# Performance work log

Measured on AMD Instinct MI355X. Metric: run time of the kernel, lower is better.

Reference implementation:

```python
import jax, jax.numpy as jnp
import numpy as np


def setup_inputs() -> dict:
    key = jax.random.key(0)
    ks = jax.random.split(key, 5)
    B, C, H, W = 32, 2048, 14, 14
    K = 113  # num_concepts + 1
    NUM_CLASSES = 200
    x = jax.random.normal(ks[0], (B, C, H, W), dtype=jnp.float32)
    concepts = jax.random.normal(ks[1], (K, C), dtype=jnp.float32)
    # small init scale for linear heads (keeps sigmoid/logits in a sane range)
    concept_fc_w = jax.random.normal(ks[2], (1, C), dtype=jnp.float32) * 0.02
    concept_fc_b = jnp.zeros((1,), dtype=jnp.float32)
    label_fc_w = jax.random.normal(ks[3], (NUM_CLASSES, C), dtype=jnp.float32) * 0.02
    label_fc_b = jnp.zeros((NUM_CLASSES,), dtype=jnp.float32)
    return {
        "x": x,
        "concepts": concepts,
        "concept_fc_w": concept_fc_w,
        "concept_fc_b": concept_fc_b,
        "label_fc_w": label_fc_w,
        "label_fc_b": label_fc_b,
    }


def reference(x, concepts, concept_fc_w, concept_fc_b, label_fc_w, label_fc_b):
    b, c, h, w = x.shape
    h2, w2 = h * 2, w * 2
    # F.interpolate(mode='bilinear', align_corners=False) == jax.image.resize bilinear
    x = jax.image.resize(x, (b, c, h2, w2), method="bilinear")
    xe = x.reshape(b, c, h2 * w2).transpose(0, 2, 1)  # [b, n, c]
    # cdist(concepts, xe, p=2) via matmul expansion (matches torch's mm-based cdist)
    x_sq = jnp.sum(xe * xe, axis=-1)                    # [b, n]
    c_sq = jnp.sum(concepts * concepts, axis=-1)        # [k]
    dots = jnp.einsum("kc,bnc->bkn", concepts, xe)      # [b, k, n]
    d2 = c_sq[None, :, None] + x_sq[:, None, :] - 2.0 * dots
    dists = jnp.sqrt(jnp.maximum(d2, 0.0))              # [b, k, n]
    attn = jax.nn.softmax(-dists, axis=1)               # softmax over concepts
    score_maps = attn.reshape(b, -1, h2, w2)            # [b, k, h2, w2]
    concept_vecs = jnp.einsum("bkn,bnc->bkc", attn[:, :-1, :], xe)  # [b, k-1, c]
    logits = jnp.einsum("bkc,c->bk", concept_vecs, concept_fc_w[0]) + concept_fc_b[0]
    concept_scores = jax.nn.sigmoid(logits)             # [b, k-1]
    preds = (concept_scores @ concepts[:-1, :]) @ label_fc_w.T + label_fc_b  # [b, 200]
    return score_maps, concept_scores, preds
```

## Files before the change

kernel.cpp:

```cpp
#include <hip/hip_runtime.h>
#include <hip/hip_bf16.h>
#include <cstdint>

typedef __attribute__((ext_vector_type(8))) short short8;
typedef __attribute__((ext_vector_type(4))) float f32x4;
typedef __attribute__((ext_vector_type(16))) float f32x16;

#define BDIM 32
#define CDIM 2048
#define NPIX 196
#define HIN 14
#define N2 784
#define W2 28
#define KDIM 113
#define KC 112
#define NCLS 200
#define NBX 14
#define BNC 56
#define NSTEP 64
#define PST 224
#define GST 200
#define RDST 68
#define SSTB 60

__global__ __launch_bounds__(256) void k_prep(const float* __restrict__ concepts,
                                              const float* __restrict__ cfcw,
                                              ushort* __restrict__ cbf,
                                              float* __restrict__ csq) {
  int k = blockIdx.x, t = threadIdx.x;
  const int kt = k >> 5, row = k & 31;
  float s = 0.f;
  for (int c = t; c < CDIM; c += 256) {
    float v = (k < KDIM) ? concepts[(size_t)k * CDIM + c] : (k == KDIM ? cfcw[c] : 0.f);
    __hip_bfloat16 h = __float2bfloat16(v);
    int st = c >> 5, it = (c >> 4) & 1, g2 = (c >> 3) & 1, j = c & 7;
    cbf[(((size_t)st * 4 + kt) * 2 + it) * 512 + (g2 * 32 + row) * 8 + j] = __bfloat16_as_ushort(h);
    float vb = __bfloat162float(h);
    s = fmaf(vb, vb, s);
  }
  __shared__ float r[4];
#pragma unroll
  for (int off = 32; off > 0; off >>= 1) s += __shfl_down(s, off, 64);
  if ((t & 63) == 0) r[t >> 6] = s;
  __syncthreads();
  if (t == 0) csq[k] = r[0] + r[1] + r[2] + r[3];
}

__global__ __launch_bounds__(512, 4) void k_xt(const float* __restrict__ x,
                                               ushort* __restrict__ xt,
                                               float* __restrict__ Gpart) {
  __shared__ float P[2][32 * PST];
  const int sg = blockIdx.x, b = blockIdx.y;
  const int tid = threadIdx.x;
  const int lane = tid & 63, wv = tid >> 6;
  const int chg = tid >> 4, seg = tid & 15;
  const int p0 = seg * 13;

  const int c0a = tid / 49,           pq0 = tid - c0a * 49;
  const int c1a = (tid + 512) / 49,   pq1 = (tid + 512) - c1a * 49;
  const int c2a = (tid + 1024) / 49,  pq2 = (tid + 1024) - c2a * 49;
  const int c3a = (tid + 1536) / 49,  pq3 = (tid + 1536) - c3a * 49;

  for (int z = tid; z < 2 * 32 * 28; z += 512) {
    int buf = z / 896, r = z - buf * 896;
    int c = r / 28, j = r - c * 28;
    P[buf][c * PST + 196 + j] = 0.f;
  }

  float g[13][5];
#pragma unroll
  for (int p = 0; p < 13; ++p)
#pragma unroll
    for (int t = 0; t < 5; ++t) g[p][t] = 0.f;

  float4 q0, q1, q2, q3 = {0.f, 0.f, 0.f, 0.f};
  auto LOADQ = [&](int s) {
    const float4* src = (const float4*)(x + ((size_t)b * CDIM + s * 32) * NPIX);
    q0 = src[tid]; q1 = src[tid + 512]; q2 = src[tid + 1024];
    if (tid < 32) q3 = src[tid + 1536];
  };
  auto WRITEQ = [&](int buf) {
    float* Pb = P[buf];
    *(float4*)&Pb[c0a * PST + 4 * pq0] = q0;
    *(float4*)&Pb[c1a * PST + 4 * pq1] = q1;
    *(float4*)&Pb[c2a * PST + 4 * pq2] = q2;
    if (tid < 32) *(float4*)&Pb[c3a * PST + 4 * pq3] = q3;
  };

  LOADQ(sg * 4);
  WRITEQ(0);
  __syncthreads();

  for (int si = 0; si < 4; ++si) {
    const int s = sg * 4 + si;
    const int cur = si & 1;
    if (si < 3) LOADQ(s + 1);
#pragma unroll
    for (int pass = 0; pass < 2; ++pass) {
      int slot = tid + pass * 512;
      if (slot < 896) {
        int t = slot >> 7, r = slot & 127;
        int it = r >> 6, l = r & 63;
        int pxp = t * 32 + (l & 31);
        int row = pxp >> 4, col = pxp & 15;
        int c0 = it * 16 + (l >> 5) * 8;
        uint uu[4];
        if (col < 14) {
          int px = row * HIN + col;
#pragma unroll
          for (int p = 0; p < 4; ++p) {
            float v0 = P[cur][(c0 + 2 * p) * PST + px];
            float v1 = P[cur][(c0 + 2 * p + 1) * PST + px];
            uu[p] = (uint)__bfloat16_as_ushort(__float2bfloat16(v0)) |
                    ((uint)__bfloat16_as_ushort(__float2bfloat16(v1)) << 16);
          }
        } else {
          uu[0] = uu[1] = uu[2] = uu[3] = 0u;
        }
        uint4 pk; pk.x = uu[0]; pk.y = uu[1]; pk.z = uu[2]; pk.w = uu[3];
        *(uint4*)&xt[((((size_t)b * 7 + t) * 64 + s) * 1024) + it * 512 + (size_t)l * 8] = pk;
      }
    }
    {
      float xv[28];
      const float* Pr = &P[cur][chg * PST];
#pragma unroll
      for (int i = 0; i < 7; ++i) *(float4*)&xv[4 * i] = *(const float4*)&Pr[p0 + 4 * i];
#pragma unroll
      for (int p = 0; p < 13; ++p) {
        float a = xv[p];
        g[p][0] = fmaf(a, a, g[p][0]);
        g[p][1] = fmaf(a, xv[p + 1], g[p][1]);
        g[p][2] = fmaf(a, xv[p + 13], g[p][2]);
        g[p][3] = fmaf(a, xv[p + 14], g[p][3]);
        g[p][4] = fmaf(a, xv[p + 15], g[p][4]);
      }
    }
    if (si < 3) WRITEQ((si + 1) & 1);
    __syncthreads();
  }

  float* Gw = &P[0][0];
#pragma unroll
  for (int p = 0; p < 13; ++p)
#pragma unroll
    for (int t = 0; t < 5; ++t) {
      float v = g[p][t];
      v += __shfl_xor(v, 16, 64);
      v += __shfl_xor(v, 32, 64);
      g[p][t] = v;
    }
  if (lane < 16) {
#pragma unroll
    for (int p = 0; p < 13; ++p)
#pragma unroll
      for (int t = 0; t < 5; ++t) Gw[((size_t)wv * 16 + lane) * 65 + p * 5 + t] = g[p][t];
  }
  __syncthreads();
#pragma unroll
  for (int it = 0; it < 2; ++it) {
    int slot = tid + it * 512;
    if (slot < 16 * 65) {
      int sseg = slot / 65, i = slot - sseg * 65;
      float v = 0.f;
#pragma unroll
      for (int ww = 0; ww < 8; ++ww) v += Gw[((size_t)ww * 16 + sseg) * 65 + i];
      int pl = i / 5, ty = i - pl * 5;
      int px = sseg * 13 + pl;
      if (px < NPIX)
        Gpart[((size_t)b * 16 + sg) * (5 * GST) + ty * GST + px] = v;
    }
  }
}

__global__ __launch_bounds__(256) void k_gred(const float* __restrict__ Gpart,
                                              float* __restrict__ Gs) {
  const int b = blockIdx.x, tid = threadIdx.x;
  for (int i = tid; i < 5 * GST; i += 256) {
    float v = 0.f;
#pragma unroll
    for (int sg = 0; sg < 16; ++sg) v += Gpart[((size_t)b * 16 + sg) * (5 * GST) + i];
    Gs[(size_t)b * (5 * GST) + i] = v;
  }
}

__global__ __launch_bounds__(256, 3) void k_gemm3(
    const ushort* __restrict__ xt,
    const ushort* __restrict__ cbf,
    const float* __restrict__ Gs,
    const float* __restrict__ csq,
    float* __restrict__ attn_out,
    float* __restrict__ part)
{
  __shared__ float RDs[128 * RDST];
  __shared__ ushort Ssb[KDIM * SSTB];
  __shared__ float csq_s[KDIM];
  __shared__ float xsqs[BNC], projs2[BNC];

  const int tid = threadIdx.x;
  const int wgid = blockIdx.x;
  const int xcd = wgid & 7, slot = wgid >> 3;
  const int bq = slot / NBX, bx = slot - bq * NBX;
  const int b = xcd + 8 * bq;
  const int n0 = bx * BNC;
  const int lane = tid & 63, w = tid >> 6;

  int r0 = bx - 1; if (r0 < 0) r0 = 0; if (r0 > 11) r0 = 11;
  const int T0 = r0 >> 1;

  if (tid < KDIM) csq_s[tid] = csq[tid];

  const ushort* abp = cbf + w * 1024 + lane * 8;
  const ushort* xtb = xt + (((size_t)b * 7 + T0) << 16) + lane * 8;

  f32x16 acc[2];
#pragma unroll
  for (int tt = 0; tt < 2; ++tt)
#pragma unroll
    for (int r = 0; r < 16; ++r) acc[tt][r] = 0.f;

#define LOADSET(A_, B_, S_)                                              \
  do {                                                                   \
    const size_t so_ = (size_t)(S_) * 4096;                              \
    const size_t xo_ = (size_t)(S_) * 1024;                              \
    A_[0] = *(const uint4*)(abp + so_);                                  \
    A_[1] = *(const uint4*)(abp + so_ + 512);                            \
    B_[0][0] = *(const uint4*)(xtb + xo_);                               \
    B_[0][1] = *(const uint4*)(xtb + xo_ + 512);                         \
    B_[1][0] = *(const uint4*)(xtb + 65536 + xo_);                       \
    B_[1][1] = *(const uint4*)(xtb + 65536 + xo_ + 512);                 \
  } while (0)

#define COMPUTE(A_, B_)                                                  \
  do {                                                                   \
    _Pragma("unroll")                                                    \
    for (int it_ = 0; it_ < 2; ++it_) {                                  \
      short8 af_ = *(const short8*)&A_[it_];                             \
      acc[0] = __builtin_amdgcn_mfma_f32_32x32x16_bf16(                  \
          af_, *(const short8*)&B_[0][it_], acc[0], 0, 0, 0);            \
      acc[1] = __builtin_amdgcn_mfma_f32_32x32x16_bf16(                  \
          af_, *(const short8*)&B_[1][it_], acc[1], 0, 0, 0);            \
    }                                                                    \
  } while (0)

  uint4 a0[2], a1[2], b0[2][2], b1[2][2];
  LOADSET(a0, b0, 0);
  for (int s = 0; s < NSTEP; s += 2) {
    if (s + 1 < NSTEP) LOADSET(a1, b1, s + 1);
    COMPUTE(a0, b0);
    if (s + 2 < NSTEP) LOADSET(a0, b0, s + 2);
    COMPUTE(a1, b1);
  }
#undef LOADSET
#undef COMPUTE

#pragma unroll
  for (int tt = 0; tt < 2; ++tt)
#pragma unroll
    for (int r = 0; r < 16; ++r) {
      int row = w * 32 + (r & 3) + 8 * (r >> 2) + 4 * (lane >> 5);
      RDs[row * RDST + tt * 32 + (lane & 31)] = acc[tt][r];
    }
  __syncthreads();

  auto COLW = [&](int col, int& p1, int& p3, int& p1g, int& p3g,
                  float& w00, float& w01, float& w10, float& w11) {
    const int i2 = 2 * bx + (col >= 28 ? 1 : 0);
    const int j2 = col - (col >= 28 ? 28 : 0);
    float si = 0.5f * i2 - 0.25f, sj = 0.5f * j2 - 0.25f;
    float fif = floorf(si), fjf = floorf(sj);
    int ii = (int)fif, jj = (int)fjf;
    float fi = si - fif, fj = sj - fjf;
    int ia = ii < 0 ? 0 : ii; int ib = (ii + 1 > 13) ? 13 : ii + 1;
    int ja = jj < 0 ? 0 : jj; int jb = (jj + 1 > 13) ? 13 : jj + 1;
    w00 = (1.f - fi) * (1.f - fj); w01 = (1.f - fi) * fj;
    w10 = fi * (1.f - fj);         w11 = fi * fj;
    if (ib == ia) { w00 += w10; w01 += w11; w10 = 0.f; w11 = 0.f; }
    if (jb == ja) { w00 += w01; w10 += w11; w01 = 0.f; w11 = 0.f; }
    p1g = ia * HIN + ja; p3g = ib * HIN + ja;
    p1 = ia * 16 + ja - T0 * 32; p3 = ib * 16 + ja - T0 * 32;
  };

  if (tid < BNC) {
    int p1, p3, p1g, p3g; float w00, w01, w10, w11;
    COLW(tid, p1, p3, p1g, p3g, w00, w01, w10, w11);
    const float* Gb = Gs + (size_t)b * (5 * GST);
    const float* Gd = Gb, *Gr = Gb + GST, *Gy = Gb + 2 * GST, *Gv = Gb + 3 * GST, *Gx = Gb + 4 * GST;
    float xsq = w00 * w00 * Gd[p1g] + w01 * w01 * Gd[p1g + 1]
              + w10 * w10 * Gd[p3g] + w11 * w11 * Gd[p3g + 1]
              + 2.f * (w00 * w01 * Gr[p1g] + w10 * w11 * Gr[p3g]
                     + w00 * w10 * Gv[p1g] + w01 * w11 * Gv[p1g + 1]
                     + w00 * w11 * Gx[p1g] + w01 * w10 * Gy[p1g + 1]);
    const float* rp = &RDs[113 * RDST];
    float pj = w00 * rp[p1] + w01 * rp[p1 + 1] + w10 * rp[p3] + w11 * rp[p3 + 1];
    xsqs[tid] = xsq; projs2[tid] = pj;
  }
  __syncthreads();

  if (tid < BNC * 4) {
    const int col = tid >> 2, sub = tid & 3;
    int p1, p3, p1g, p3g; float w00, w01, w10, w11;
    COLW(col, p1, p3, p1g, p3g, w00, w01, w10, w11);
    const float xq = xsqs[col];
    float ev[29];
    float mx = -1e30f;
#pragma unroll
    for (int i = 0; i < 29; ++i) {
      int k = sub + 4 * i;
      if (k < KDIM) {
        const float* rk = &RDs[k * RDST];
        float dot = w00 * rk[p1] + w01 * rk[p1 + 1] + w10 * rk[p3] + w11 * rk[p3 + 1];
        float d2 = csq_s[k] + xq - 2.f * dot;
        float sv = -sqrtf(fmaxf(d2, 0.f));
        ev[i] = sv;
        mx = fmaxf(mx, sv);
      }
    }
    mx = fmaxf(mx, __shfl_xor(mx, 1, 64));
    mx = fmaxf(mx, __shfl_xor(mx, 2, 64));
    float ssum = 0.f;
#pragma unroll
    for (int i = 0; i < 29; ++i) {
      int k = sub + 4 * i;
      if (k < KDIM) {
        float e = __expf(ev[i] - mx);
        ev[i] = e;
        Ssb[k * SSTB + col] = __bfloat16_as_ushort(__float2bfloat16(e));
        ssum += e;
      }
    }
    ssum += __shfl_xor(ssum, 1, 64);
    ssum += __shfl_xor(ssum, 2, 64);
    const float rinv = 1.f / ssum;
    float* op = attn_out + (size_t)b * KDIM * N2 + n0 + col;
#pragma unroll
    for (int i = 0; i < 29; ++i) {
      int k = sub + 4 * i;
      if (k < KDIM) op[(size_t)k * N2] = ev[i] * rinv;
    }
    if (sub == 0) projs2[col] *= rinv;
  }
  __syncthreads();

  if (tid < KC * 2) {
    const int k = tid >> 1, s2 = tid & 1;
    float lg = 0.f;
    for (int c2 = s2; c2 < BNC; c2 += 2)
      lg = fmaf(__uint_as_float((uint)Ssb[k * SSTB + c2] << 16), projs2[c2], lg);
    lg += __shfl_xor(lg, 1, 64);
    if (s2 == 0) part[((size_t)b * NBX + bx) * KC + k] = lg;
  }
}

__global__ __launch_bounds__(256) void k_tmp(
    const float* __restrict__ concepts, const float* __restrict__ part,
    const float* __restrict__ cfcb, float* __restrict__ cs_out,
    float* __restrict__ tmp) {
  __shared__ float cs_s[KC];
  const int b = blockIdx.y, cx = blockIdx.x;
  const int t = threadIdx.x;
  if (t < KC) {
    float l = cfcb[0];
#pragma unroll
    for (int q = 0; q < NBX; ++q) l += part[((size_t)b * NBX + q) * KC + t];
    float csv = 1.f / (1.f + __expf(-l));
    cs_s[t] = csv;
    if (cx == 0) cs_out[b * KC + t] = csv;
  }
  __syncthreads();
  const int c = cx * 256 + t;
  float a = 0.f;
#pragma unroll 8
  for (int k = 0; k < KC; ++k) a = fmaf(cs_s[k], concepts[(size_t)k * CDIM + c], a);
  tmp[(size_t)b * CDIM + c] = a;
}

__global__ __launch_bounds__(256) void k_pred2(
    const float* __restrict__ labw, const float* __restrict__ labb,
    const float* __restrict__ tmp, float* __restrict__ preds) {
  const int w = blockIdx.x * 4 + (threadIdx.x >> 6);
  const int lane = threadIdx.x & 63;
  const int b = w / NCLS, cls = w % NCLS;
  if (b >= BDIM) return;
  const float* tr = tmp + (size_t)b * CDIM;
  const float* wr = labw + (size_t)cls * CDIM;
  float a = 0.f;
#pragma unroll
  for (int c0 = 0; c0 < CDIM; c0 += 256) {
    float4 t = *(const float4*)&tr[c0 + lane * 4];
    float4 v = *(const float4*)&wr[c0 + lane * 4];
    a += t.x * v.x + t.y * v.y + t.z * v.z + t.w * v.w;
  }
#pragma unroll
  for (int off = 32; off > 0; off >>= 1) a += __shfl_down(a, off, 64);
  if (lane == 0) preds[b * NCLS + cls] = a + labb[cls];
}

extern "C" void kernel_launch(void* const* d_in, const int* in_sizes, int n_in,
                              void* d_out, int out_size, void* d_ws, size_t ws_size,
                              hipStream_t stream) {
  const float* x        = (const float*)d_in[0];
  const float* concepts = (const float*)d_in[1];
  const float* cfcw     = (const float*)d_in[2];
  const float* cfcb     = (const float*)d_in[3];
  const float* labw     = (const float*)d_in[4];
  const float* labb     = (const float*)d_in[5];

  float* out    = (float*)d_out;
  float* sm_out = out;
  float* cs_out = out + (size_t)BDIM * KDIM * N2;
  float* pr_out = cs_out + (size_t)BDIM * KC;

  char* ws = (char*)d_ws;
  float*  csq   = (float*)(ws + 0);
  float*  part  = (float*)(ws + 512);
  ushort* cbf   = (ushort*)(ws + 201216);
  float*  tmp   = (float*)(ws + 725504);
  float*  Gpart = (float*)(ws + 987648);
  float*  Gs    = (float*)(ws + 3035648);
  ushort* xt    = (ushort*)(ws + 3163648);

  k_prep <<<dim3(128), dim3(256), 0, stream>>>(concepts, cfcw, cbf, csq);
  k_xt   <<<dim3(16, BDIM), dim3(512), 0, stream>>>(x, xt, Gpart);
  k_gred <<<dim3(BDIM), dim3(256), 0, stream>>>(Gpart, Gs);
  k_gemm3<<<dim3(448), dim3(256), 0, stream>>>(xt, cbf, Gs, csq, sm_out, part);
  k_tmp  <<<dim3(CDIM / 256, BDIM), dim3(256), 0, stream>>>(concepts, part, cfcb, cs_out, tmp);
  k_pred2<<<dim3((BDIM * NCLS + 3) / 4), dim3(256), 0, stream>>>(labw, labb, tmp, pr_out);
}
```

Measured before the change: 84.64 us.

## Merge prep and transpose kernels, fold G reduction into GEMM, deepen load pipeline

Combines the concept-prep and x-transpose kernels into one launch by giving extra workgroups the prep work. It drops the separate G-reduction kernel, so the GEMM kernel sums the 16 partials itself when it computes xsq. The GEMM main loop now prefetches four stages of registers instead of two. These changes cut two kernel launches and their sync points, and hide more global-load latency. In exchange the GEMM does more scattered global reads in its epilogue, and the deeper prefetch raises register pressure, which could lower occupancy. The stage kernel's launch bounds also drop from 4 to 2 blocks per CU.

```diff
diff --git a/kernel.cpp b/kernel.cpp
--- a/kernel.cpp
+++ b/kernel.cpp
@@ -23,36 +23,46 @@
 #define RDST 68
 #define SSTB 60
 
-__global__ __launch_bounds__(256) void k_prep(const float* __restrict__ concepts,
-                                              const float* __restrict__ cfcw,
-                                              ushort* __restrict__ cbf,
-                                              float* __restrict__ csq) {
-  int k = blockIdx.x, t = threadIdx.x;
-  const int kt = k >> 5, row = k & 31;
-  float s = 0.f;
-  for (int c = t; c < CDIM; c += 256) {
-    float v = (k < KDIM) ? concepts[(size_t)k * CDIM + c] : (k == KDIM ? cfcw[c] : 0.f);
-    __hip_bfloat16 h = __float2bfloat16(v);
-    int st = c >> 5, it = (c >> 4) & 1, g2 = (c >> 3) & 1, j = c & 7;
-    cbf[(((size_t)st * 4 + kt) * 2 + it) * 512 + (g2 * 32 + row) * 8 + j] = __bfloat16_as_ushort(h);
-    float vb = __bfloat162float(h);
-    s = fmaf(vb, vb, s);
-  }
-  __shared__ float r[4];
-#pragma unroll
-  for (int off = 32; off > 0; off >>= 1) s += __shfl_down(s, off, 64);
-  if ((t & 63) == 0) r[t >> 6] = s;
-  __syncthreads();
-  if (t == 0) csq[k] = r[0] + r[1] + r[2] + r[3];
-}
-
-__global__ __launch_bounds__(512, 4) void k_xt(const float* __restrict__ x,
-                                               ushort* __restrict__ xt,
-                                               float* __restrict__ Gpart) {
+__global__ __launch_bounds__(512, 2) void k_stage(
+    const float* __restrict__ x,
+    const float* __restrict__ concepts,
+    const float* __restrict__ cfcw,
+    ushort* __restrict__ cbf,
+    float* __restrict__ csq,
+    ushort* __restrict__ xt,
+    float* __restrict__ Gpart) {
   __shared__ float P[2][32 * PST];
-  const int sg = blockIdx.x, b = blockIdx.y;
+  __shared__ float r8[8];
+  const int wgid = blockIdx.x;
   const int tid = threadIdx.x;
   const int lane = tid & 63, wv = tid >> 6;
+
+  if (wgid >= 512) {
+    const int k = wgid - 512;
+    const int kt = k >> 5, row = k & 31;
+    float s = 0.f;
+    for (int c = tid; c < CDIM; c += 512) {
+      float v = (k < KDIM) ? concepts[(size_t)k * CDIM + c] : (k == KDIM ? cfcw[c] : 0.f);
+      __hip_bfloat16 h = __float2bfloat16(v);
+      int st = c >> 5, it = (c >> 4) & 1, g2 = (c >> 3) & 1, j = c & 7;
+      cbf[(((size_t)st * 4 + kt) * 2 + it) * 512 + (g2 * 32 + row) * 8 + j] = __bfloat16_as_ushort(h);
+      float vb = __bfloat162float(h);
+      s = fmaf(vb, vb, s);
+    }
+#pragma unroll
+    for (int off = 32; off > 0; off >>= 1) s += __shfl_down(s, off, 64);
+    if (lane == 0) r8[wv] = s;
+    __syncthreads();
+    if (tid == 0) {
+      float tot = 0.f;
+#pragma unroll
+      for (int i = 0; i < 8; ++i) tot += r8[i];
+      csq[k] = tot;
+    }
+    return;
+  }
+
+  const int sg = wgid & 15, b = wgid >> 4;
   const int chg = tid >> 4, seg = tid & 15;
   const int p0 = seg * 13;
 
@@ -173,21 +183,10 @@
   }
 }
 
-__global__ __launch_bounds__(256) void k_gred(const float* __restrict__ Gpart,
-                                              float* __restrict__ Gs) {
-  const int b = blockIdx.x, tid = threadIdx.x;
-  for (int i = tid; i < 5 * GST; i += 256) {
-    float v = 0.f;
-#pragma unroll
-    for (int sg = 0; sg < 16; ++sg) v += Gpart[((size_t)b * 16 + sg) * (5 * GST) + i];
-    Gs[(size_t)b * (5 * GST) + i] = v;
-  }
-}
-
 __global__ __launch_bounds__(256, 3) void k_gemm3(
     const ushort* __restrict__ xt,
     const ushort* __restrict__ cbf,
-    const float* __restrict__ Gs,
+    const float* __restrict__ Gpart,
     const float* __restrict__ csq,
     float* __restrict__ attn_out,
     float* __restrict__ part)
@@ -243,13 +242,17 @@
     }                                                                    \
   } while (0)
 
-  uint4 a0[2], a1[2], b0[2][2], b1[2][2];
-  LOADSET(a0, b0, 0);
-  for (int s = 0; s < NSTEP; s += 2) {
-    if (s + 1 < NSTEP) LOADSET(a1, b1, s + 1);
-    COMPUTE(a0, b0);
-    if (s + 2 < NSTEP) LOADSET(a0, b0, s + 2);
-    COMPUTE(a1, b1);
+  uint4 aA[2], aB[2], aC[2], aD[2];
+  uint4 bA[2][2], bB[2][2], bC[2][2], bD[2][2];
+  LOADSET(aA, bA, 0);
+  LOADSET(aB, bB, 1);
+  LOADSET(aC, bC, 2);
+  LOADSET(aD, bD, 3);
+  for (int s = 0; s < NSTEP; s += 4) {
+    COMPUTE(aA, bA); if (s + 4 < NSTEP) LOADSET(aA, bA, s + 4);
+    COMPUTE(aB, bB); if (s + 5 < NSTEP) LOADSET(aB, bB, s + 5);
+    COMPUTE(aC, bC); if (s + 6 < NSTEP) LOADSET(aC, bC, s + 6);
+    COMPUTE(aD, bD); if (s + 7 < NSTEP) LOADSET(aD, bD, s + 7);
   }
 #undef LOADSET
 #undef COMPUTE
@@ -284,13 +287,18 @@
   if (tid < BNC) {
     int p1, p3, p1g, p3g; float w00, w01, w10, w11;
     COLW(tid, p1, p3, p1g, p3g, w00, w01, w10, w11);
-    const float* Gb = Gs + (size_t)b * (5 * GST);
-    const float* Gd = Gb, *Gr = Gb + GST, *Gy = Gb + 2 * GST, *Gv = Gb + 3 * GST, *Gx = Gb + 4 * GST;
-    float xsq = w00 * w00 * Gd[p1g] + w01 * w01 * Gd[p1g + 1]
-              + w10 * w10 * Gd[p3g] + w11 * w11 * Gd[p3g + 1]
-              + 2.f * (w00 * w01 * Gr[p1g] + w10 * w11 * Gr[p3g]
-                     + w00 * w10 * Gv[p1g] + w01 * w11 * Gv[p1g + 1]
-                     + w00 * w11 * Gx[p1g] + w01 * w10 * Gy[p1g + 1]);
+    const float* Gp = Gpart + (size_t)b * 16 * (5 * GST);
+    auto GS = [&](int ty, int px) {
+      float v = 0.f;
+#pragma unroll
+      for (int sg = 0; sg < 16; ++sg) v += Gp[(size_t)sg * (5 * GST) + ty * GST + px];
+      return v;
+    };
+    float xsq = w00 * w00 * GS(0, p1g) + w01 * w01 * GS(0, p1g + 1)
+              + w10 * w10 * GS(0, p3g) + w11 * w11 * GS(0, p3g + 1)
+              + 2.f * (w00 * w01 * GS(1, p1g) + w10 * w11 * GS(1, p3g)
+                     + w00 * w10 * GS(3, p1g) + w01 * w11 * GS(3, p1g + 1)
+                     + w00 * w11 * GS(4, p1g) + w01 * w10 * GS(2, p1g + 1));
     const float* rp = &RDs[113 * RDST];
     float pj = w00 * rp[p1] + w01 * rp[p1 + 1] + w10 * rp[p3] + w11 * rp[p3 + 1];
     xsqs[tid] = xsq; projs2[tid] = pj;
@@ -417,13 +425,10 @@
   ushort* cbf   = (ushort*)(ws + 201216);
   float*  tmp   = (float*)(ws + 725504);
   float*  Gpart = (float*)(ws + 987648);
-  float*  Gs    = (float*)(ws + 3035648);
   ushort* xt    = (ushort*)(ws + 3163648);
 
-  k_prep <<<dim3(128), dim3(256), 0, stream>>>(concepts, cfcw, cbf, csq);
-  k_xt   <<<dim3(16, BDIM), dim3(512), 0, stream>>>(x, xt, Gpart);
-  k_gred <<<dim3(BDIM), dim3(256), 0, stream>>>(Gpart, Gs);
-  k_gemm3<<<dim3(448), dim3(256), 0, stream>>>(xt, cbf, Gs, csq, sm_out, part);
+  k_stage<<<dim3(640), dim3(512), 0, stream>>>(x, concepts, cfcw, cbf, csq, xt, Gpart);
+  k_gemm3<<<dim3(448), dim3(256), 0, stream>>>(xt, cbf, Gpart, csq, sm_out, part);
   k_tmp  <<<dim3(CDIM / 256, BDIM), dim3(256), 0, stream>>>(concepts, part, cfcb, cs_out, tmp);
   k_pred2<<<dim3((BDIM * NCLS + 3) / 4), dim3(256), 0, stream>>>(labw, labb, tmp, pr_out);
 }
```

Result: slower. 87.94 us (+3.9%).
